# Optimization experiments

Measured on AMD Instinct MI355X. Metric: run time of the kernel, lower is better.

## Reference

```python
import jax, jax.numpy as jnp
import numpy as np

VOCAB = 32000
DIM = 1024
LAYERS = 4
B = 4
L = 1024


def setup_inputs() -> dict:
    key = jax.random.key(0)
    ks = jax.random.split(key, 5)
    input_ids = jax.random.randint(ks[0], (B, L), 0, VOCAB)
    embed = jax.random.normal(ks[1], (VOCAB, DIM), jnp.float32) * 0.02
    # 1/sqrt(fan_in) scaling keeps the recurrent state numerically stable over L steps
    W = jax.random.normal(ks[2], (LAYERS, 2 * DIM, 2 * DIM), jnp.float32) * (1.0 / np.sqrt(2 * DIM))
    out_w = jax.random.normal(ks[3], (VOCAB, DIM), jnp.float32) * 0.02
    starter = jax.random.normal(ks[4], (LAYERS, DIM), jnp.float32) * 0.02
    return {"input_ids": input_ids, "embed": embed, "W": W, "out_w": out_w, "starter": starter}


def reference(input_ids, embed, W, out_w, starter):
    Bsz, Lsz = input_ids.shape
    d = starter.shape[1]
    x = embed[input_ids]  # [B, L, d]
    # initial per-layer state, broadcast over batch: [layers, B, d]
    s0 = jnp.broadcast_to(starter[:, None, :], (W.shape[0], Bsz, d))

    def time_step(s_stack, x_t):
        # s_stack: [layers, B, d], x_t: [B, d]
        def layer_step(h, ws):
            Wi, si = ws  # Wi: [2d, 2d], si: [B, d]
            out = jnp.concatenate([h, si], axis=-1) @ Wi.T  # [B, 2d]
            h_new, s_new = jnp.split(out, 2, axis=-1)
            return h_new, s_new
        y, new_s = jax.lax.scan(layer_step, x_t, (W, s_stack))
        return new_s, y

    _, ys = jax.lax.scan(time_step, s0, jnp.swapaxes(x, 0, 1))  # ys: [L, B, d]
    logits = jnp.einsum('lbd,vd->blv', ys, out_w)  # [B, L, vocab]
    return logits
```

## Files before the change

### kernel.cpp

```cpp
#include <hip/hip_runtime.h>
#include <hip/hip_bf16.h>
#include <stdint.h>

#define BATCH 4
#define SEQ 1024
#define DIMX 1024
#define VOCAB 32000
#define NLAYERS 4
#define NBLK 256

#define W_GARR 4096
#define W_GREL 4608
#define W_LREL 4864
#define W_FLAG 5120

using bf16x8 = __attribute__((ext_vector_type(8))) short;
using f32x4v = __attribute__((ext_vector_type(4))) float;

__device__ __forceinline__ uint16_t f2b(float f) {
  __hip_bfloat16 h = __float2bfloat16(f);
  return *reinterpret_cast<uint16_t*>(&h);
}
__device__ __forceinline__ float b2f(uint16_t u) {
  __hip_bfloat16 h = *reinterpret_cast<__hip_bfloat16*>(&u);
  return __bfloat162float(h);
}
__device__ __forceinline__ void fsplit(float v, uint16_t& h, uint16_t& l) {
  h = f2b(v);
  l = f2b(v - b2f(h));
}

__device__ __forceinline__ uint32_t get_xcc() {
  uint32_t x;
  asm volatile("s_getreg_b32 %0, hwreg(HW_REG_XCC_ID)" : "=s"(x));
  return x & 7u;
}

__global__ __launch_bounds__(256) void k_embed_split(const int* __restrict__ ids,
                                                     const float* __restrict__ emb,
                                                     uint16_t* __restrict__ Hhi,
                                                     uint16_t* __restrict__ Hlo) {
  int idx = blockIdx.x * 256 + threadIdx.x;
  int d4 = idx & (DIMX / 4 - 1);
  int tb = idx >> 8;
  int t = tb >> 2, b = tb & 3;
  int id = ids[b * SEQ + t];
  float4 v = reinterpret_cast<const float4*>(emb + (size_t)id * DIMX)[d4];
  ushort4 h, l;
  fsplit(v.x, h.x, l.x); fsplit(v.y, h.y, l.y); fsplit(v.z, h.z, l.z); fsplit(v.w, h.w, l.w);
  reinterpret_cast<ushort4*>(Hhi)[idx] = h;
  reinterpret_cast<ushort4*>(Hlo)[idx] = l;
}

__global__ __launch_bounds__(256) void k_split_w(const float* __restrict__ W,
                                                 uint16_t* __restrict__ W1h, uint16_t* __restrict__ W1l,
                                                 uint16_t* __restrict__ WSh, uint16_t* __restrict__ WSl,
                                                 uint16_t* __restrict__ M1h, uint16_t* __restrict__ M1l) {
  int idx = blockIdx.x * 256 + threadIdx.x;
  int c4 = idx & 255;
  int row = idx >> 8;
  int l = row >> 12, r = row & 4095;
  const float* Wl = W + (size_t)l * 4 * 1024 * 1024;
  const float* src;
  uint16_t *dh, *dl;
  size_t doff;
  if (r < 2048) { src = Wl + (size_t)r * 2048; dh = W1h; dl = W1l; doff = ((size_t)l * 2048 + r) * 1024; }
  else if (r < 3072) { int rr = r - 2048; src = Wl + (size_t)rr * 2048 + 1024; dh = WSh; dl = WSl; doff = ((size_t)l * 1024 + rr) * 1024; }
  else { int rr = r - 3072; src = Wl + (size_t)(1024 + rr) * 2048 + 1024; dh = M1h; dl = M1l; doff = ((size_t)l * 1024 + rr) * 1024; }
  float4 v = reinterpret_cast<const float4*>(src)[c4];
  ushort4 h, lo4;
  fsplit(v.x, h.x, lo4.x); fsplit(v.y, h.y, lo4.y); fsplit(v.z, h.z, lo4.z); fsplit(v.w, h.w, lo4.w);
  reinterpret_cast<ushort4*>(dh + doff)[c4] = h;
  reinterpret_cast<ushort4*>(dl + doff)[c4] = lo4;
}

__global__ __launch_bounds__(256) void k_trans_w(const float* __restrict__ W,
                                                 uint16_t* __restrict__ T1h, uint16_t* __restrict__ T1l) {
  __shared__ float t[64][65];
  int l = blockIdx.z;
  const float* Wl = W + (size_t)l * 4 * 1024 * 1024;
  int i0 = blockIdx.y * 64, j0 = blockIdx.x * 64;
  int c4 = (threadIdx.x & 15) * 4, rr = threadIdx.x >> 4;
#pragma unroll
  for (int p = 0; p < 4; ++p) {
    int r = rr + p * 16;
    float4 v = *reinterpret_cast<const float4*>(Wl + (size_t)(1024 + i0 + r) * 2048 + 1024 + j0 + c4);
    t[r][c4] = v.x; t[r][c4 + 1] = v.y; t[r][c4 + 2] = v.z; t[r][c4 + 3] = v.w;
  }
  __syncthreads();
#pragma unroll
  for (int p = 0; p < 4; ++p) {
    int j = rr + p * 16;
    ushort4 h, l4;
    fsplit(t[c4 + 0][j], h.x, l4.x);
    fsplit(t[c4 + 1][j], h.y, l4.y);
    fsplit(t[c4 + 2][j], h.z, l4.z);
    fsplit(t[c4 + 3][j], h.w, l4.w);
    size_t o = (size_t)l * 1024 * 1024 + (size_t)(j0 + j) * 1024 + i0 + c4;
    *reinterpret_cast<ushort4*>(T1h + o) = h;
    *reinterpret_cast<ushort4*>(T1l + o) = l4;
  }
}

template <int BM, int BN>
__global__ __launch_bounds__(256) void k_mfma(
    int K,
    const uint16_t* __restrict__ Ahi, const uint16_t* __restrict__ Alo, int a_cs, int a_bs, size_t a_z,
    const uint16_t* __restrict__ Bhi, const uint16_t* __restrict__ Blo, int ldb, size_t b_z,
    const float* __restrict__ ADD, int add_cs, int add_bs,
    float* __restrict__ O1f, int o1_cs, int o1_bs,
    uint16_t* __restrict__ O1hi, uint16_t* __restrict__ O1lo, int o1s_cs, int o1s_bs, int split_n0, size_t o1_z,
    uint16_t* __restrict__ O2hi, uint16_t* __restrict__ O2lo, int o2_cs, int o2_bs, size_t o2_z) {
  constexpr int FM = BM / 32;
  constexpr int FN = BN / 32;
  __shared__ uint16_t sAh[BM * 32], sAl[BM * 32], sBh[BN * 32], sBl[BN * 32];
  size_t zb = blockIdx.z;
  Ahi += zb * a_z; Alo += zb * a_z;
  Bhi += zb * b_z; Blo += zb * b_z;
  if (O1hi) { O1hi += zb * o1_z; O1lo += zb * o1_z; }
  if (O2hi) { O2hi += zb * o2_z; O2lo += zb * o2_z; }
  int tid = threadIdx.x;
  int lane = tid & 63;
  int wave = tid >> 6;
  int wm = wave >> 1, wn = wave & 1;
  int m0 = blockIdx.y * BM, n0 = blockIdx.x * BN;
  f32x4v acc[FM][FN] = {};
  for (int kt = 0; kt < K; kt += 32) {
    __syncthreads();
#pragma unroll
    for (int q = 0; q < BM / 64; ++q) {
      int off = q * 4096 + tid * 16;
      int r = off >> 6;
      int cu = (off & 63) >> 1;
      size_t goff = (size_t)(m0 / 4 + (r >> 2)) * a_cs + (size_t)(r & 3) * a_bs + kt + cu;
      __builtin_amdgcn_global_load_lds(
          (const __attribute__((address_space(1))) uint32_t*)(Ahi + goff),
          (__attribute__((address_space(3))) uint32_t*)((char*)sAh + off), 16, 0, 0);
      __builtin_amdgcn_global_load_lds(
          (const __attribute__((address_space(1))) uint32_t*)(Alo + goff),
          (__attribute__((address_space(3))) uint32_t*)((char*)sAl + off), 16, 0, 0);
    }
#pragma unroll
    for (int q = 0; q < BN / 64; ++q) {
      int off = q * 4096 + tid * 16;
      int r = off >> 6, cu = (off & 63) >> 1;
      size_t goff = (size_t)(n0 + r) * ldb + kt + cu;
      __builtin_amdgcn_global_load_lds(
          (const __attribute__((address_space(1))) uint32_t*)(Bhi + goff),
          (__attribute__((address_space(3))) uint32_t*)((char*)sBh + off), 16, 0, 0);
      __builtin_amdgcn_global_load_lds(
          (const __attribute__((address_space(1))) uint32_t*)(Blo + goff),
          (__attribute__((address_space(3))) uint32_t*)((char*)sBl + off), 16, 0, 0);
    }
    __syncthreads();
    int rsel = lane & 15, ko = (lane >> 4) * 8;
    bf16x8 ah[FM], al[FM], bh[FN], bl[FN];
#pragma unroll
    for (int mf = 0; mf < FM; ++mf) {
      int row = wm * (FM * 16) + mf * 16 + rsel;
      ah[mf] = *reinterpret_cast<const bf16x8*>(sAh + row * 32 + ko);
      al[mf] = *reinterpret_cast<const bf16x8*>(sAl + row * 32 + ko);
    }
#pragma unroll
    for (int nf = 0; nf < FN; ++nf) {
      int row = wn * (FN * 16) + nf * 16 + rsel;
      bh[nf] = *reinterpret_cast<const bf16x8*>(sBh + row * 32 + ko);
      bl[nf] = *reinterpret_cast<const bf16x8*>(sBl + row * 32 + ko);
    }
#pragma unroll
    for (int mf = 0; mf < FM; ++mf)
#pragma unroll
      for (int nf = 0; nf < FN; ++nf) {
        acc[mf][nf] = __builtin_amdgcn_mfma_f32_16x16x32_bf16(ah[mf], bh[nf], acc[mf][nf], 0, 0, 0);
        acc[mf][nf] = __builtin_amdgcn_mfma_f32_16x16x32_bf16(ah[mf], bl[nf], acc[mf][nf], 0, 0, 0);
        acc[mf][nf] = __builtin_amdgcn_mfma_f32_16x16x32_bf16(al[mf], bh[nf], acc[mf][nf], 0, 0, 0);
      }
  }
  int rowg = (lane >> 4) * 4, colg = lane & 15;
#pragma unroll
  for (int mf = 0; mf < FM; ++mf)
#pragma unroll
    for (int nf = 0; nf < FN; ++nf)
#pragma unroll
      for (int r = 0; r < 4; ++r) {
        int m = m0 + wm * (FM * 16) + mf * 16 + rowg + r;
        int n = n0 + wn * (FN * 16) + nf * 16 + colg;
        size_t ro = (size_t)(m >> 2);
        float dot = acc[mf][nf][r];
        float v = dot;
        if (ADD) v += ADD[ro * add_cs + (size_t)(m & 3) * add_bs + n];
        if (O1f) O1f[ro * o1_cs + (size_t)(m & 3) * o1_bs + n] = v;
        if (O1hi && n >= split_n0) {
          uint16_t h, l;
          fsplit(v, h, l);
          size_t o = ro * o1s_cs + (size_t)(m & 3) * o1s_bs + (n - split_n0);
          O1hi[o] = h; O1lo[o] = l;
        }
        if (O2hi) {
          uint16_t h, l;
          fsplit(dot, h, l);
          size_t o = (o2_bs == 0) ? ((size_t)n * o2_cs + m)
                                  : (ro * o2_cs + (size_t)(m & 3) * o2_bs + n);
          O2hi[o] = h; O2lo[o] = l;
        }
      }
}

__device__ __forceinline__ void gbar(uint32_t* S, int flat, uint32_t& gen) {
  __syncthreads();
  gen++;
  int bid = blockIdx.x;
  if (flat) {
    if (threadIdx.x == 0)
      __hip_atomic_store(S + (size_t)bid * 16, gen, __ATOMIC_RELEASE, __HIP_MEMORY_SCOPE_AGENT);
    if (bid == 0) {
      while (__hip_atomic_load(S + (size_t)threadIdx.x * 16, __ATOMIC_RELAXED, __HIP_MEMORY_SCOPE_AGENT) < gen)
        __builtin_amdgcn_s_sleep(2);
      __syncthreads();
      if (threadIdx.x == 0) {
        __builtin_amdgcn_fence(__ATOMIC_ACQUIRE, "agent");
        __hip_atomic_store(S + W_GREL, gen, __ATOMIC_RELEASE, __HIP_MEMORY_SCOPE_AGENT);
      }
      __syncthreads();
    } else {
      if (threadIdx.x == 0) {
        while (__hip_atomic_load(S + W_GREL, __ATOMIC_RELAXED, __HIP_MEMORY_SCOPE_AGENT) < gen)
          __builtin_amdgcn_s_sleep(2);
        __builtin_amdgcn_fence(__ATOMIC_ACQUIRE, "agent");
      }
      __syncthreads();
    }
  } else {
    int xcd = bid & 7, q = bid >> 3;
    if (q != 0) {
      if (threadIdx.x == 0) {
        asm volatile("s_waitcnt vmcnt(0)" ::: "memory");
        __hip_atomic_store(S + (size_t)(xcd * 32 + q) * 16, gen, __ATOMIC_RELAXED, __HIP_MEMORY_SCOPE_AGENT);
        while (__hip_atomic_load(S + W_LREL + xcd * 16, __ATOMIC_RELAXED, __HIP_MEMORY_SCOPE_AGENT) < gen)
          __builtin_amdgcn_s_sleep(1);
        asm volatile("buffer_inv sc0" ::: "memory");
      }
      __builtin_amdgcn_sched_barrier(0);
      __syncthreads();
    } else {
      if (threadIdx.x < 31) {
        uint32_t* s = S + (size_t)(xcd * 32 + 1 + threadIdx.x) * 16;
        while (__hip_atomic_load(s, __ATOMIC_RELAXED, __HIP_MEMORY_SCOPE_AGENT) < gen)
          __builtin_amdgcn_s_sleep(1);
      }
      __syncthreads();
      if (threadIdx.x == 0)
        __hip_atomic_store(S + W_GARR + xcd * 16, gen, __ATOMIC_RELEASE, __HIP_MEMORY_SCOPE_AGENT);
      if (xcd == 0) {
        if (threadIdx.x < 8) {
          while (__hip_atomic_load(S + W_GARR + threadIdx.x * 16, __ATOMIC_RELAXED, __HIP_MEMORY_SCOPE_AGENT) < gen)
            __builtin_amdgcn_s_sleep(1);
        }
        __syncthreads();
        if (threadIdx.x == 0)
          __hip_atomic_store(S + W_GREL, gen, __ATOMIC_RELEASE, __HIP_MEMORY_SCOPE_AGENT);
      }
      if (threadIdx.x == 0) {
        while (__hip_atomic_load(S + W_GREL, __ATOMIC_RELAXED, __HIP_MEMORY_SCOPE_AGENT) < gen)
          __builtin_amdgcn_s_sleep(1);
        __builtin_amdgcn_fence(__ATOMIC_ACQUIRE, "agent");
        __hip_atomic_store(S + W_LREL + xcd * 16, gen, __ATOMIC_RELEASE, __HIP_MEMORY_SCOPE_AGENT);
      }
      __builtin_amdgcn_sched_barrier(0);
      __syncthreads();
    }
  }
}

__device__ __forceinline__ f32x4v wtile16(
    const uint16_t* __restrict__ Ah, const uint16_t* __restrict__ Al,
    int a_cs, int a_bs, int m0,
    const uint16_t* __restrict__ Bh, const uint16_t* __restrict__ Bl,
    int n0, int lane) {
  int rsel = lane & 15, ko = (lane >> 4) * 8;
  int am = m0 + rsel;
  const uint16_t* pah = Ah + (size_t)(am >> 2) * a_cs + (size_t)(am & 3) * a_bs + ko;
  const uint16_t* pal = Al + (size_t)(am >> 2) * a_cs + (size_t)(am & 3) * a_bs + ko;
  const uint16_t* pbh = Bh + (size_t)(n0 + rsel) * 1024 + ko;
  const uint16_t* pbl = Bl + (size_t)(n0 + rsel) * 1024 + ko;
  f32x4v acc = {0.f, 0.f, 0.f, 0.f};
#pragma unroll 4
  for (int kt = 0; kt < 1024; kt += 32) {
    bf16x8 ah = *reinterpret_cast<const bf16x8*>(pah + kt);
    bf16x8 al = *reinterpret_cast<const bf16x8*>(pal + kt);
    bf16x8 bh = *reinterpret_cast<const bf16x8*>(pbh + kt);
    bf16x8 bl = *reinterpret_cast<const bf16x8*>(pbl + kt);
    acc = __builtin_amdgcn_mfma_f32_16x16x32_bf16(ah, bh, acc, 0, 0, 0);
    acc = __builtin_amdgcn_mfma_f32_16x16x32_bf16(ah, bl, acc, 0, 0, 0);
    acc = __builtin_amdgcn_mfma_f32_16x16x32_bf16(al, bh, acc, 0, 0, 0);
  }
  return acc;
}

__device__ __forceinline__ f32x4v wtile16_lds(
    const uint16_t* __restrict__ Ah, const uint16_t* __restrict__ Al,
    int a_cs, int a_bs, int m0,
    const uint16_t* sBh, const uint16_t* sBl,
    int lane) {
  int rsel = lane & 15, ko = (lane >> 4) * 8;
  int am = m0 + rsel;
  const uint16_t* pah = Ah + (size_t)(am >> 2) * a_cs + (size_t)(am & 3) * a_bs + ko;
  const uint16_t* pal = Al + (size_t)(am >> 2) * a_cs + (size_t)(am & 3) * a_bs + ko;
  int rb = rsel * 1024;
  int s7 = rsel & 7;
  f32x4v acc0 = {0.f, 0.f, 0.f, 0.f}, acc1 = {0.f, 0.f, 0.f, 0.f};
#pragma unroll 4
  for (int kt = 0; kt < 1024; kt += 64) {
    int e0 = kt + ko, e1 = kt + 32 + ko;
    int o0 = rb + ((((e0) >> 3) ^ s7) << 3);
    int o1 = rb + ((((e1) >> 3) ^ s7) << 3);
    bf16x8 ah0 = *reinterpret_cast<const bf16x8*>(pah + kt);
    bf16x8 al0 = *reinterpret_cast<const bf16x8*>(pal + kt);
    bf16x8 ah1 = *reinterpret_cast<const bf16x8*>(pah + kt + 32);
    bf16x8 al1 = *reinterpret_cast<const bf16x8*>(pal + kt + 32);
    bf16x8 bh0 = *reinterpret_cast<const bf16x8*>(sBh + o0);
    bf16x8 bl0 = *reinterpret_cast<const bf16x8*>(sBl + o0);
    bf16x8 bh1 = *reinterpret_cast<const bf16x8*>(sBh + o1);
    bf16x8 bl1 = *reinterpret_cast<const bf16x8*>(sBl + o1);
    acc0 = __builtin_amdgcn_mfma_f32_16x16x32_bf16(ah0, bh0, acc0, 0, 0, 0);
    acc1 = __builtin_amdgcn_mfma_f32_16x16x32_bf16(ah1, bh1, acc1, 0, 0, 0);
    acc0 = __builtin_amdgcn_mfma_f32_16x16x32_bf16(ah0, bl0, acc0, 0, 0, 0);
    acc1 = __builtin_amdgcn_mfma_f32_16x16x32_bf16(ah1, bl1, acc1, 0, 0, 0);
    acc0 = __builtin_amdgcn_mfma_f32_16x16x32_bf16(al0, bh0, acc0, 0, 0, 0);
    acc1 = __builtin_amdgcn_mfma_f32_16x16x32_bf16(al1, bh1, acc1, 0, 0, 0);
  }
  return acc0 + acc1;
}

__global__ __launch_bounds__(256) void k_layer(
    uint32_t* S,
    float* __restrict__ P,
    uint16_t* __restrict__ PUh, uint16_t* __restrict__ PUl,
    uint16_t* __restrict__ Sh, uint16_t* __restrict__ Sl,
    const uint16_t* __restrict__ M1h, const uint16_t* __restrict__ M1l,
    const uint16_t* __restrict__ M16h, const uint16_t* __restrict__ M16l,
    const uint16_t* __restrict__ M128h, const uint16_t* __restrict__ M128l,
    uint16_t* G3h0, uint16_t* G3l0, uint16_t* G3h1, uint16_t* G3l1,
    uint16_t* BEh, uint16_t* BEl,
    float* LAMf, uint16_t* LAMh, uint16_t* LAMl,
    uint16_t* GSh0, uint16_t* GSl0, uint16_t* GSh1, uint16_t* GSl1,
    const float* __restrict__ starterL) {
  __shared__ uint16_t sB[2][32 * 1024];
  int tid = threadIdx.x, bid = blockIdx.x;
  int lane = tid & 63;
  int wv = tid >> 6;
  int xcd = bid & 7;
  int q = bid >> 3;
  uint32_t gen = 0;
  int rowg = (lane >> 4) * 4, colg = lane & 15;

  int nt13 = xcd * 8 + (q & 7);
  int m0_13 = ((q >> 3) * 4 + wv) * 16;
  int n0_13 = nt13 * 16;
  int m0_2 = (wv & 1) * 16;
  int nt2 = xcd * 8 + q * 2 + (wv >> 1);
  int n0_2 = nt2 * 16;
  int lrb2 = (wv >> 1) * 16 * 1024;
  int n0_b = (xcd * 8 + q * 4 + wv) * 16;

  {
    int idx = bid * 256 + tid;
    if (idx < BATCH * DIMX) {
      int b = idx >> 10, d = idx & 1023;
      float v = starterL[d];
      uint16_t h, l;
      fsplit(v, h, l);
      size_t o = (size_t)b * 1024 + d;
      BEh[o] = h; BEl[o] = l;
      G3h0[o] = h; G3l0[o] = l;
      GSh0[o] = h; GSl0[o] = l;
      Sh[o] = h; Sl[o] = l;
    }
  }

  if (threadIdx.x == 0 && get_xcc() != (uint32_t)xcd)
    __hip_atomic_store(S + W_FLAG, 1u, __ATOMIC_RELAXED, __HIP_MEMORY_SCOPE_AGENT);
  gbar(S, 1, gen);
  int flat = (int)__hip_atomic_load(S + W_FLAG, __ATOMIC_RELAXED, __HIP_MEMORY_SCOPE_AGENT);

  {
    const uint16_t* gh = M1h + (size_t)n0_13 * 1024;
    const uint16_t* gl = M1l + (size_t)n0_13 * 1024;
    for (int i = tid; i < 16 * 128; i += 256) {
      int r = i >> 7, c8 = i & 127;
      int dst = r * 1024 + ((c8 ^ (r & 7)) << 3);
      *reinterpret_cast<bf16x8*>(&sB[0][dst]) = *reinterpret_cast<const bf16x8*>(gh + (size_t)r * 1024 + c8 * 8);
      *reinterpret_cast<bf16x8*>(&sB[1][dst]) = *reinterpret_cast<const bf16x8*>(gl + (size_t)r * 1024 + c8 * 8);
    }
  }
  __syncthreads();

  for (int j = 1; j < 16; ++j) {
    {
      f32x4v acc = wtile16_lds(PUh + (size_t)(j - 1) * 4096, PUl + (size_t)(j - 1) * 4096,
                               65536, 1024, m0_13, &sB[0][0], &sB[1][0], lane);
      int n = n0_13 + colg;
#pragma unroll
      for (int rr = 0; rr < 4; ++rr) {
        int m = m0_13 + rowg + rr;
        int c = m >> 2, b = m & 3;
        size_t t = (size_t)(c * 16 + j);
        float* pu = P + (t * 4 + b) * 2048 + 1024 + n;
        float v = acc[rr] + *pu;
        *pu = v;
        uint16_t h, l;
        fsplit(v, h, l);
        size_t o = (t * 4 + b) * 1024 + n;
        PUh[o] = h; PUl[o] = l;
      }
    }
    gbar(S, flat, gen);
  }

  {
    int idx = bid * 256 + tid;
    if (idx < 32 * 1024) {
      int r = idx >> 10, d = idx & 1023;
      int g = r >> 2, b = r & 3;
      float v = P[((size_t)(g * 128 + 15) * 4 + b) * 2048 + 1024 + d];
      LAMf[idx] = v;
      uint16_t h, l;
      fsplit(v, h, l);
      LAMh[idx] = h; LAMl[idx] = l;
    }
  }
  gbar(S, flat, gen);

  if (q < 4) {
    int nb = (xcd * 8 + q * 2) * 16;
    const uint16_t* gh = M16h + (size_t)nb * 1024;
    const uint16_t* gl = M16l + (size_t)nb * 1024;
    for (int i = tid; i < 32 * 128; i += 256) {
      int r = i >> 7, c8 = i & 127;
      int dst = r * 1024 + ((c8 ^ (r & 7)) << 3);
      *reinterpret_cast<bf16x8*>(&sB[0][dst]) = *reinterpret_cast<const bf16x8*>(gh + (size_t)r * 1024 + c8 * 8);
      *reinterpret_cast<bf16x8*>(&sB[1][dst]) = *reinterpret_cast<const bf16x8*>(gl + (size_t)r * 1024 + c8 * 8);
    }
  }
  __syncthreads();

  for (int j = 1; j < 8; ++j) {
    if (q < 4) {
      f32x4v acc = wtile16_lds(LAMh + (size_t)(j - 1) * 32768, LAMl + (size_t)(j - 1) * 32768,
                               4096, 1024, m0_2, &sB[0][lrb2], &sB[1][lrb2], lane);
      int n = n0_2 + colg;
#pragma unroll
      for (int rr = 0; rr < 4; ++rr) {
        int m = m0_2 + rowg + rr;
        int g = m >> 2, b = m & 3;
        int c = 8 * g + j;
        float e = P[((size_t)(c * 16 + 15) * 4 + b) * 2048 + 1024 + n];
        float v = acc[rr] + e;
        size_t o = (size_t)j * 32768 + (size_t)m * 1024 + n;
        LAMf[o] = v;
        uint16_t h, l;
        fsplit(v, h, l);
        LAMh[o] = h; LAMl[o] = l;
      }
    }
    gbar(S, flat, gen);
  }

  for (int g = 0; g < 7; ++g) {
    if (q < 2) {
      f32x4v acc = wtile16(BEh + (size_t)g * 16384, BEl + (size_t)g * 16384,
                           4096, 1024, 0, M128h, M128l, n0_b, lane);
      if ((lane >> 4) == 0) {
        int n = n0_b + colg;
#pragma unroll
        for (int rr = 0; rr < 4; ++rr) {
          int b = rr;
          float v = acc[rr] + LAMf[(size_t)7 * 32768 + (size_t)(g * 4 + b) * 1024 + n];
          uint16_t h, l;
          fsplit(v, h, l);
          size_t ob = (size_t)(g + 1) * 16384 + (size_t)b * 1024 + n;
          BEh[ob] = h; BEl[ob] = l;
          int c = 8 * (g + 1);
          size_t o1 = (size_t)(c * 4 + b) * 1024 + n;
          G3h0[o1] = h; G3l0[o1] = l;
          size_t o2 = ((size_t)(c * 16) * 4 + b) * 1024 + n;
          Sh[o2] = h; Sl[o2] = l;
          size_t o3 = (size_t)((g + 1) * 4 + b) * 1024 + n;
          GSh0[o3] = h; GSl0[o3] = l;
        }
      }
    }
    gbar(S, flat, gen);
  }

  int gsc = 0;
  for (int j = 1; j < 8; ++j) {
    uint16_t* gih = gsc ? GSh1 : GSh0;
    uint16_t* gil = gsc ? GSl1 : GSl0;
    uint16_t* goh = gsc ? GSh0 : GSh1;
    uint16_t* gol = gsc ? GSl0 : GSl1;
    if (q < 4) {
      f32x4v acc = wtile16_lds(gih, gil, 4096, 1024, m0_2, &sB[0][lrb2], &sB[1][lrb2], lane);
      int n = n0_2 + colg;
#pragma unroll
      for (int rr = 0; rr < 4; ++rr) {
        int m = m0_2 + rowg + rr;
        int g = m >> 2, b = m & 3;
        int c = 8 * g + j;
        float lam = LAMf[(size_t)(j - 1) * 32768 + (size_t)m * 1024 + n];
        float v = acc[rr] + lam;
        uint16_t h, l;
        fsplit(v, h, l);
        size_t o1 = (size_t)(c * 4 + b) * 1024 + n;
        G3h0[o1] = h; G3l0[o1] = l;
        size_t o2 = ((size_t)(c * 16) * 4 + b) * 1024 + n;
        Sh[o2] = h; Sl[o2] = l;
        uint16_t h2, l2;
        fsplit(acc[rr], h2, l2);
        goh[(size_t)m * 1024 + n] = h2;
        gol[(size_t)m * 1024 + n] = l2;
      }
    }
    gbar(S, flat, gen);
    gsc ^= 1;
  }

  {
    const uint16_t* gh = M1h + (size_t)n0_13 * 1024;
    const uint16_t* gl = M1l + (size_t)n0_13 * 1024;
    for (int i = tid; i < 16 * 128; i += 256) {
      int r = i >> 7, c8 = i & 127;
      int dst = r * 1024 + ((c8 ^ (r & 7)) << 3);
      *reinterpret_cast<bf16x8*>(&sB[0][dst]) = *reinterpret_cast<const bf16x8*>(gh + (size_t)r * 1024 + c8 * 8);
      *reinterpret_cast<bf16x8*>(&sB[1][dst]) = *reinterpret_cast<const bf16x8*>(gl + (size_t)r * 1024 + c8 * 8);
    }
  }
  __syncthreads();

  int g3 = 0;
  for (int j = 1; j < 16; ++j) {
    uint16_t* gih = g3 ? G3h1 : G3h0;
    uint16_t* gil = g3 ? G3l1 : G3l0;
    uint16_t* goh = g3 ? G3h0 : G3h1;
    uint16_t* gol = g3 ? G3l0 : G3l1;
    {
      f32x4v acc = wtile16_lds(gih, gil, 4096, 1024, m0_13, &sB[0][0], &sB[1][0], lane);
      int n = n0_13 + colg;
#pragma unroll
      for (int rr = 0; rr < 4; ++rr) {
        int m = m0_13 + rowg + rr;
        int c = m >> 2, b = m & 3;
        float u = P[((size_t)(c * 16 + j - 1) * 4 + b) * 2048 + 1024 + n];
        float v = acc[rr] + u;
        uint16_t h, l;
        fsplit(v, h, l);
        size_t o = ((size_t)(c * 16 + j) * 4 + b) * 1024 + n;
        Sh[o] = h; Sl[o] = l;
        uint16_t h2, l2;
        fsplit(acc[rr], h2, l2);
        goh[(size_t)m * 1024 + n] = h2;
        gol[(size_t)m * 1024 + n] = l2;
      }
    }
    if (j < 15) gbar(S, flat, gen);
    g3 ^= 1;
  }
}

__global__ __launch_bounds__(256) void k_reorder_hi(const uint16_t* __restrict__ Hhi, uint16_t* __restrict__ Y) {
  int idx = blockIdx.x * 256 + threadIdx.x;
  int d4 = idx & (DIMX / 4 - 1);
  int tb = idx >> 8;
  int t = tb >> 2, b = tb & 3;
  ushort4 v = reinterpret_cast<const ushort4*>(Hhi)[idx];
  reinterpret_cast<ushort4*>(Y + (size_t)(b * SEQ + t) * DIMX)[d4] = v;
}

__global__ __launch_bounds__(256) void k_cast_w(const float* __restrict__ src, uint16_t* __restrict__ dst, int n4) {
  int idx = blockIdx.x * 256 + threadIdx.x;
  if (idx >= n4) return;
  float4 v = reinterpret_cast<const float4*>(src)[idx];
  ushort4 o;
  o.x = f2b(v.x); o.y = f2b(v.y); o.z = f2b(v.z); o.w = f2b(v.w);
  reinterpret_cast<ushort4*>(dst)[idx] = o;
}

__global__ __launch_bounds__(256) void k_logits(const uint16_t* __restrict__ A,
                                                const uint16_t* __restrict__ Bt,
                                                float* __restrict__ C) {
  __shared__ uint16_t As[128 * 32];
  __shared__ uint16_t Bs[128 * 32];
  int tid = threadIdx.x;
  int bx = blockIdx.x, by = blockIdx.y;
  int lane = tid & 63, wave = tid >> 6;
  int wm = wave >> 1, wn = wave & 1;
  f32x4v acc[4][4] = {};
  const uint16_t* Ag = A + (size_t)by * 128 * 1024;
  const uint16_t* Bg = Bt + (size_t)bx * 128 * 1024;
  for (int kt = 0; kt < 1024; kt += 32) {
    __syncthreads();
#pragma unroll
    for (int q = 0; q < 2; ++q) {
      int off = q * 4096 + tid * 16;
      int r = off >> 6, cu = (off & 63) >> 1;
      __builtin_amdgcn_global_load_lds(
          (const __attribute__((address_space(1))) uint32_t*)(Ag + (size_t)r * 1024 + kt + cu),
          (__attribute__((address_space(3))) uint32_t*)((char*)As + off), 16, 0, 0);
      __builtin_amdgcn_global_load_lds(
          (const __attribute__((address_space(1))) uint32_t*)(Bg + (size_t)r * 1024 + kt + cu),
          (__attribute__((address_space(3))) uint32_t*)((char*)Bs + off), 16, 0, 0);
    }
    __syncthreads();
    int rsel = lane & 15, ko = (lane >> 4) * 8;
    bf16x8 af[4], bfr[4];
#pragma unroll
    for (int mf = 0; mf < 4; ++mf)
      af[mf] = *reinterpret_cast<const bf16x8*>(As + (wm * 64 + mf * 16 + rsel) * 32 + ko);
#pragma unroll
    for (int nf = 0; nf < 4; ++nf)
      bfr[nf] = *reinterpret_cast<const bf16x8*>(Bs + (wn * 64 + nf * 16 + rsel) * 32 + ko);
#pragma unroll
    for (int mf = 0; mf < 4; ++mf)
#pragma unroll
      for (int nf = 0; nf < 4; ++nf)
        acc[mf][nf] = __builtin_amdgcn_mfma_f32_16x16x32_bf16(af[mf], bfr[nf], acc[mf][nf], 0, 0, 0);
  }
  int rowg = (lane >> 4) * 4;
  int colg = lane & 15;
#pragma unroll
  for (int mf = 0; mf < 4; ++mf)
#pragma unroll
    for (int nf = 0; nf < 4; ++nf)
#pragma unroll
      for (int r = 0; r < 4; ++r) {
        int m = by * 128 + wm * 64 + mf * 16 + rowg + r;
        int n = bx * 128 + wn * 64 + nf * 16 + colg;
        C[(size_t)m * VOCAB + n] = acc[mf][nf][r];
      }
}

extern "C" void kernel_launch(void* const* d_in, const int* in_sizes, int n_in,
                              void* d_out, int out_size, void* d_ws, size_t ws_size,
                              hipStream_t stream) {
  const int* ids = (const int*)d_in[0];
  const float* emb = (const float*)d_in[1];
  const float* W = (const float*)d_in[2];
  const float* outw = (const float*)d_in[3];
  const float* starter = (const float*)d_in[4];
  float* out = (float*)d_out;

  char* wsb = (char*)d_ws;
  size_t off = 0;
  auto alloc = [&](size_t bytes) {
    void* p = wsb + off;
    off = (off + bytes + 255) & ~(size_t)255;
    return p;
  };
  const size_t TB = SEQ * BATCH;
  const size_t MB1 = (size_t)1024 * 1024;

  uint32_t* SYNC = (uint32_t*)alloc((size_t)NLAYERS * 8192 * 4);
  uint16_t* Hh[2] = {(uint16_t*)alloc(TB * DIMX * 2), (uint16_t*)alloc(TB * DIMX * 2)};
  uint16_t* Hl[2] = {(uint16_t*)alloc(TB * DIMX * 2), (uint16_t*)alloc(TB * DIMX * 2)};
  float* P = (float*)alloc(TB * 2 * DIMX * 4);
  uint16_t* PUh = (uint16_t*)alloc(TB * DIMX * 2);
  uint16_t* PUl = (uint16_t*)alloc(TB * DIMX * 2);
  uint16_t* Sh = (uint16_t*)alloc(TB * DIMX * 2);
  uint16_t* Sl = (uint16_t*)alloc(TB * DIMX * 2);
  uint16_t* W1h = (uint16_t*)alloc((size_t)NLAYERS * 2048 * 1024 * 2);
  uint16_t* W1l = (uint16_t*)alloc((size_t)NLAYERS * 2048 * 1024 * 2);
  uint16_t* WSh = (uint16_t*)alloc((size_t)NLAYERS * MB1 * 2);
  uint16_t* WSl = (uint16_t*)alloc((size_t)NLAYERS * MB1 * 2);
  uint16_t* M1h = (uint16_t*)alloc((size_t)NLAYERS * MB1 * 2);
  uint16_t* M1l = (uint16_t*)alloc((size_t)NLAYERS * MB1 * 2);
  uint16_t* T1h = (uint16_t*)alloc((size_t)NLAYERS * MB1 * 2);
  uint16_t* T1l = (uint16_t*)alloc((size_t)NLAYERS * MB1 * 2);
  uint16_t* M16Ah = (uint16_t*)alloc((size_t)NLAYERS * MB1 * 2);
  uint16_t* M16Al = (uint16_t*)alloc((size_t)NLAYERS * MB1 * 2);
  uint16_t* M128Ah = (uint16_t*)alloc((size_t)NLAYERS * MB1 * 2);
  uint16_t* M128Al = (uint16_t*)alloc((size_t)NLAYERS * MB1 * 2);
  uint16_t* G3h0 = (uint16_t*)alloc((size_t)256 * 1024 * 2);
  uint16_t* G3l0 = (uint16_t*)alloc((size_t)256 * 1024 * 2);
  uint16_t* G3h1 = (uint16_t*)alloc((size_t)256 * 1024 * 2);
  uint16_t* G3l1 = (uint16_t*)alloc((size_t)256 * 1024 * 2);
  uint16_t* BEh = (uint16_t*)alloc((size_t)8 * 16 * 1024 * 2);
  uint16_t* BEl = (uint16_t*)alloc((size_t)8 * 16 * 1024 * 2);
  float* LAMf = (float*)alloc((size_t)8 * 32 * 1024 * 4);
  uint16_t* LAMh = (uint16_t*)alloc((size_t)8 * 32 * 1024 * 2);
  uint16_t* LAMl = (uint16_t*)alloc((size_t)8 * 32 * 1024 * 2);
  uint16_t* GSh0 = (uint16_t*)alloc((size_t)32 * 1024 * 2);
  uint16_t* GSl0 = (uint16_t*)alloc((size_t)32 * 1024 * 2);
  uint16_t* GSh1 = (uint16_t*)alloc((size_t)32 * 1024 * 2);
  uint16_t* GSl1 = (uint16_t*)alloc((size_t)32 * 1024 * 2);
  uint16_t* YSB = (uint16_t*)alloc(TB * DIMX * 2);
  uint16_t* OWB = (uint16_t*)alloc((size_t)VOCAB * DIMX * 2);

  uint16_t* CMh[2] = {(uint16_t*)P, Sh};
  uint16_t* CMl[2] = {(uint16_t*)P + 4 * MB1, Sl};
  uint16_t* CTh[2] = {(uint16_t*)P + 8 * MB1, Hh[1]};
  uint16_t* CTl[2] = {(uint16_t*)P + 12 * MB1, Hl[1]};

  hipMemsetAsync(SYNC, 0, (size_t)NLAYERS * 8192 * 4, stream);
  k_split_w<<<NLAYERS * 4096, 256, 0, stream>>>(W, W1h, W1l, WSh, WSl, M1h, M1l);
  k_trans_w<<<dim3(16, 16, NLAYERS), 256, 0, stream>>>(W, T1h, T1l);
  k_cast_w<<<(int)((size_t)VOCAB * DIMX / 4 / 256), 256, 0, stream>>>(outw, OWB, VOCAB * DIMX / 4);
  k_embed_split<<<(int)(TB * DIMX / 4 / 256), 256, 0, stream>>>(ids, emb, Hh[0], Hl[0]);

  {
    const uint16_t *inMh = M1h, *inMl = M1l, *inTh = T1h, *inTl = T1l;
    for (int k = 1; k <= 7; ++k) {
      uint16_t *oMh, *oMl;
      if (k == 4) { oMh = M16Ah; oMl = M16Al; }
      else if (k == 7) { oMh = M128Ah; oMl = M128Al; }
      else { oMh = CMh[k & 1]; oMl = CMl[k & 1]; }
      uint16_t* oTh = (k < 7) ? CTh[k & 1] : nullptr;
      uint16_t* oTl = (k < 7) ? CTl[k & 1] : nullptr;
      k_mfma<128, 128><<<dim3(8, 8, NLAYERS), 256, 0, stream>>>(
          1024,
          inMh, inMl, 4096, 1024, MB1,
          inTh, inTl, 1024, MB1,
          nullptr, 0, 0,
          nullptr, 0, 0,
          oMh, oMl, 4096, 1024, 0, MB1,
          oTh, oTl, 1024, 0, MB1);
      inMh = oMh; inMl = oMl; inTh = oTh; inTl = oTl;
    }
  }

  int cur = 0;
  for (int l = 0; l < NLAYERS; ++l) {
    k_mfma<128, 128><<<dim3(16, 32, 1), 256, 0, stream>>>(
        1024,
        Hh[cur], Hl[cur], 4096, 1024, 0,
        W1h + (size_t)l * 2048 * 1024, W1l + (size_t)l * 2048 * 1024, 1024, 0,
        nullptr, 0, 0,
        P, 8192, 2048,
        PUh, PUl, 4096, 1024, 1024, 0,
        nullptr, nullptr, 0, 1, 0);

    k_layer<<<NBLK, 256, 0, stream>>>(
        SYNC + (size_t)l * 8192,
        P, PUh, PUl, Sh, Sl,
        M1h + (size_t)l * MB1, M1l + (size_t)l * MB1,
        M16Ah + (size_t)l * MB1, M16Al + (size_t)l * MB1,
        M128Ah + (size_t)l * MB1, M128Al + (size_t)l * MB1,
        G3h0, G3l0, G3h1, G3l1,
        BEh, BEl, LAMf, LAMh, LAMl,
        GSh0, GSl0, GSh1, GSl1,
        starter + (size_t)l * DIMX);

    k_mfma<128, 128><<<dim3(8, 32, 1), 256, 0, stream>>>(
        1024,
        Sh, Sl, 4096, 1024, 0,
        WSh + (size_t)l * MB1, WSl + (size_t)l * MB1, 1024, 0,
        P, 8192, 2048,
        nullptr, 0, 0,
        Hh[cur ^ 1], Hl[cur ^ 1], 4096, 1024, 0, 0,
        nullptr, nullptr, 0, 1, 0);
    cur ^= 1;
  }

  k_reorder_hi<<<(int)(TB * DIMX / 4 / 256), 256, 0, stream>>>(Hh[cur], YSB);
  k_logits<<<dim3(VOCAB / 128, TB / 128), 256, 0, stream>>>(YSB, OWB, out);
}
```

Measured before the change: 4.229 ms.

## Localize scan stages per XCD and use XCD-local barriers between steps

```diff
diff --git a/kernel.cpp b/kernel.cpp
--- a/kernel.cpp
+++ b/kernel.cpp
@@ -206,35 +206,36 @@
       }
 }
 
-__device__ __forceinline__ void gbar(uint32_t* S, int flat, uint32_t& gen) {
+__device__ __forceinline__ void bar_any(uint32_t* S, int flat, int global, uint32_t& gen) {
+  gen++;
   __syncthreads();
-  gen++;
-  int bid = blockIdx.x;
+  int bid = blockIdx.x, tid = threadIdx.x;
   if (flat) {
-    if (threadIdx.x == 0)
+    if (tid == 0)
       __hip_atomic_store(S + (size_t)bid * 16, gen, __ATOMIC_RELEASE, __HIP_MEMORY_SCOPE_AGENT);
     if (bid == 0) {
-      while (__hip_atomic_load(S + (size_t)threadIdx.x * 16, __ATOMIC_RELAXED, __HIP_MEMORY_SCOPE_AGENT) < gen)
+      while (__hip_atomic_load(S + (size_t)tid * 16, __ATOMIC_RELAXED, __HIP_MEMORY_SCOPE_AGENT) < gen)
         __builtin_amdgcn_s_sleep(2);
       __syncthreads();
-      if (threadIdx.x == 0) {
+      if (tid == 0) {
         __builtin_amdgcn_fence(__ATOMIC_ACQUIRE, "agent");
         __hip_atomic_store(S + W_GREL, gen, __ATOMIC_RELEASE, __HIP_MEMORY_SCOPE_AGENT);
       }
       __syncthreads();
     } else {
-      if (threadIdx.x == 0) {
+      if (tid == 0) {
         while (__hip_atomic_load(S + W_GREL, __ATOMIC_RELAXED, __HIP_MEMORY_SCOPE_AGENT) < gen)
           __builtin_amdgcn_s_sleep(2);
         __builtin_amdgcn_fence(__ATOMIC_ACQUIRE, "agent");
       }
       __syncthreads();
     }
-  } else {
-    int xcd = bid & 7, q = bid >> 3;
+    return;
+  }
+  int xcd = bid & 7, q = bid >> 3;
+  if (global) {
     if (q != 0) {
-      if (threadIdx.x == 0) {
-        asm volatile("s_waitcnt vmcnt(0)" ::: "memory");
+      if (tid == 0) {
         __hip_atomic_store(S + (size_t)(xcd * 32 + q) * 16, gen, __ATOMIC_RELAXED, __HIP_MEMORY_SCOPE_AGENT);
         while (__hip_atomic_load(S + W_LREL + xcd * 16, __ATOMIC_RELAXED, __HIP_MEMORY_SCOPE_AGENT) < gen)
           __builtin_amdgcn_s_sleep(1);
@@ -243,28 +244,52 @@
       __builtin_amdgcn_sched_barrier(0);
       __syncthreads();
     } else {
-      if (threadIdx.x < 31) {
-        uint32_t* s = S + (size_t)(xcd * 32 + 1 + threadIdx.x) * 16;
+      if (tid < 31) {
+        uint32_t* s = S + (size_t)(xcd * 32 + 1 + tid) * 16;
         while (__hip_atomic_load(s, __ATOMIC_RELAXED, __HIP_MEMORY_SCOPE_AGENT) < gen)
           __builtin_amdgcn_s_sleep(1);
       }
       __syncthreads();
-      if (threadIdx.x == 0)
+      if (tid == 0)
         __hip_atomic_store(S + W_GARR + xcd * 16, gen, __ATOMIC_RELEASE, __HIP_MEMORY_SCOPE_AGENT);
       if (xcd == 0) {
-        if (threadIdx.x < 8) {
-          while (__hip_atomic_load(S + W_GARR + threadIdx.x * 16, __ATOMIC_RELAXED, __HIP_MEMORY_SCOPE_AGENT) < gen)
+        if (tid < 8) {
+          while (__hip_atomic_load(S + W_GARR + tid * 16, __ATOMIC_RELAXED, __HIP_MEMORY_SCOPE_AGENT) < gen)
             __builtin_amdgcn_s_sleep(1);
         }
         __syncthreads();
-        if (threadIdx.x == 0)
+        if (tid == 0)
           __hip_atomic_store(S + W_GREL, gen, __ATOMIC_RELEASE, __HIP_MEMORY_SCOPE_AGENT);
       }
-      if (threadIdx.x == 0) {
+      if (tid == 0) {
         while (__hip_atomic_load(S + W_GREL, __ATOMIC_RELAXED, __HIP_MEMORY_SCOPE_AGENT) < gen)
           __builtin_amdgcn_s_sleep(1);
         __builtin_amdgcn_fence(__ATOMIC_ACQUIRE, "agent");
         __hip_atomic_store(S + W_LREL + xcd * 16, gen, __ATOMIC_RELEASE, __HIP_MEMORY_SCOPE_AGENT);
+      }
+      __builtin_amdgcn_sched_barrier(0);
+      __syncthreads();
+    }
+  } else {
+    if (q != 0) {
+      if (tid == 0) {
+        __hip_atomic_store(S + (size_t)(xcd * 32 + q) * 16, gen, __ATOMIC_RELAXED, __HIP_MEMORY_SCOPE_AGENT);
+        while (__hip_atomic_load(S + W_LREL + xcd * 16, __ATOMIC_RELAXED, __HIP_MEMORY_SCOPE_AGENT) < gen)
+          __builtin_amdgcn_s_sleep(1);
+        asm volatile("buffer_inv sc0" ::: "memory");
+      }
+      __builtin_amdgcn_sched_barrier(0);
+      __syncthreads();
+    } else {
+      if (tid < 31) {
+        uint32_t* s = S + (size_t)(xcd * 32 + 1 + tid) * 16;
+        while (__hip_atomic_load(s, __ATOMIC_RELAXED, __HIP_MEMORY_SCOPE_AGENT) < gen)
+          __builtin_amdgcn_s_sleep(1);
+      }
+      __syncthreads();
+      if (tid == 0) {
+        asm volatile("buffer_inv sc0" ::: "memory");
+        __hip_atomic_store(S + W_LREL + xcd * 16, gen, __ATOMIC_RELAXED, __HIP_MEMORY_SCOPE_AGENT);
       }
       __builtin_amdgcn_sched_barrier(0);
       __syncthreads();
@@ -354,14 +379,10 @@
   uint32_t gen = 0;
   int rowg = (lane >> 4) * 4, colg = lane & 15;
 
-  int nt13 = xcd * 8 + (q & 7);
-  int m0_13 = ((q >> 3) * 4 + wv) * 16;
-  int n0_13 = nt13 * 16;
-  int m0_2 = (wv & 1) * 16;
-  int nt2 = xcd * 8 + q * 2 + (wv >> 1);
-  int n0_2 = nt2 * 16;
-  int lrb2 = (wv >> 1) * 16 * 1024;
-  int n0_b = (xcd * 8 + q * 4 + wv) * 16;
+  int m0_13 = xcd * 32 + (wv & 1) * 16;
+  int n0_13 = (2 * q + (wv >> 1)) * 16;
+  int lrb13 = (wv >> 1) * 16 * 1024;
+  int n0_2 = (q * 4 + wv) * 16;
 
   {
     int idx = bid * 256 + tid;
@@ -378,15 +399,15 @@
     }
   }
 
-  if (threadIdx.x == 0 && get_xcc() != (uint32_t)xcd)
+  if (tid == 0 && get_xcc() != (uint32_t)xcd)
     __hip_atomic_store(S + W_FLAG, 1u, __ATOMIC_RELAXED, __HIP_MEMORY_SCOPE_AGENT);
-  gbar(S, 1, gen);
+  bar_any(S, 1, 1, gen);
   int flat = (int)__hip_atomic_load(S + W_FLAG, __ATOMIC_RELAXED, __HIP_MEMORY_SCOPE_AGENT);
 
   {
-    const uint16_t* gh = M1h + (size_t)n0_13 * 1024;
-    const uint16_t* gl = M1l + (size_t)n0_13 * 1024;
-    for (int i = tid; i < 16 * 128; i += 256) {
+    const uint16_t* gh = M1h + (size_t)(32 * q) * 1024;
+    const uint16_t* gl = M1l + (size_t)(32 * q) * 1024;
+    for (int i = tid; i < 32 * 128; i += 256) {
       int r = i >> 7, c8 = i & 127;
       int dst = r * 1024 + ((c8 ^ (r & 7)) << 3);
       *reinterpret_cast<bf16x8*>(&sB[0][dst]) = *reinterpret_cast<const bf16x8*>(gh + (size_t)r * 1024 + c8 * 8);
@@ -398,7 +419,7 @@
   for (int j = 1; j < 16; ++j) {
     {
       f32x4v acc = wtile16_lds(PUh + (size_t)(j - 1) * 4096, PUl + (size_t)(j - 1) * 4096,
-                               65536, 1024, m0_13, &sB[0][0], &sB[1][0], lane);
+                               65536, 1024, m0_13, &sB[0][lrb13], &sB[1][lrb13], lane);
       int n = n0_13 + colg;
 #pragma unroll
       for (int rr = 0; rr < 4; ++rr) {
@@ -414,68 +435,55 @@
         PUh[o] = h; PUl[o] = l;
       }
     }
-    gbar(S, flat, gen);
-  }
-
-  {
-    int idx = bid * 256 + tid;
-    if (idx < 32 * 1024) {
-      int r = idx >> 10, d = idx & 1023;
-      int g = r >> 2, b = r & 3;
-      float v = P[((size_t)(g * 128 + 15) * 4 + b) * 2048 + 1024 + d];
-      LAMf[idx] = v;
+    bar_any(S, flat, 0, gen);
+  }
+
+  if (q == 0) {
+    for (int i = tid; i < 4096; i += 256) {
+      int b = i >> 10, d = i & 1023;
+      float v = P[((size_t)(xcd * 128 + 15) * 4 + b) * 2048 + 1024 + d];
+      size_t o = (size_t)xcd * 16384 + (size_t)b * 1024 + d;
+      LAMf[o] = v;
       uint16_t h, l;
       fsplit(v, h, l);
-      LAMh[idx] = h; LAMl[idx] = l;
-    }
-  }
-  gbar(S, flat, gen);
-
-  if (q < 4) {
-    int nb = (xcd * 8 + q * 2) * 16;
-    const uint16_t* gh = M16h + (size_t)nb * 1024;
-    const uint16_t* gl = M16l + (size_t)nb * 1024;
-    for (int i = tid; i < 32 * 128; i += 256) {
-      int r = i >> 7, c8 = i & 127;
-      int dst = r * 1024 + ((c8 ^ (r & 7)) << 3);
-      *reinterpret_cast<bf16x8*>(&sB[0][dst]) = *reinterpret_cast<const bf16x8*>(gh + (size_t)r * 1024 + c8 * 8);
-      *reinterpret_cast<bf16x8*>(&sB[1][dst]) = *reinterpret_cast<const bf16x8*>(gl + (size_t)r * 1024 + c8 * 8);
-    }
-  }
-  __syncthreads();
+      LAMh[o] = h; LAMl[o] = l;
+    }
+  }
+  bar_any(S, flat, 0, gen);
 
   for (int j = 1; j < 8; ++j) {
-    if (q < 4) {
-      f32x4v acc = wtile16_lds(LAMh + (size_t)(j - 1) * 32768, LAMl + (size_t)(j - 1) * 32768,
-                               4096, 1024, m0_2, &sB[0][lrb2], &sB[1][lrb2], lane);
-      int n = n0_2 + colg;
-#pragma unroll
-      for (int rr = 0; rr < 4; ++rr) {
-        int m = m0_2 + rowg + rr;
-        int g = m >> 2, b = m & 3;
-        int c = 8 * g + j;
-        float e = P[((size_t)(c * 16 + 15) * 4 + b) * 2048 + 1024 + n];
-        float v = acc[rr] + e;
-        size_t o = (size_t)j * 32768 + (size_t)m * 1024 + n;
-        LAMf[o] = v;
-        uint16_t h, l;
-        fsplit(v, h, l);
-        LAMh[o] = h; LAMl[o] = l;
-      }
-    }
-    gbar(S, flat, gen);
-  }
-
-  for (int g = 0; g < 7; ++g) {
-    if (q < 2) {
-      f32x4v acc = wtile16(BEh + (size_t)g * 16384, BEl + (size_t)g * 16384,
-                           4096, 1024, 0, M128h, M128l, n0_b, lane);
-      if ((lane >> 4) == 0) {
-        int n = n0_b + colg;
+    if (q < 16) {
+      size_t abase = (size_t)(j - 1) * 131072 + (size_t)xcd * 16384;
+      f32x4v acc = wtile16(LAMh + abase, LAMl + abase, 4096, 1024, 0, M16h, M16l, n0_2, lane);
+      if (rowg == 0) {
+        int n = n0_2 + colg;
 #pragma unroll
         for (int rr = 0; rr < 4; ++rr) {
           int b = rr;
-          float v = acc[rr] + LAMf[(size_t)7 * 32768 + (size_t)(g * 4 + b) * 1024 + n];
+          int c = 8 * xcd + j;
+          float e = P[((size_t)(c * 16 + 15) * 4 + b) * 2048 + 1024 + n];
+          float v = acc[rr] + e;
+          size_t o = (size_t)j * 131072 + (size_t)xcd * 16384 + (size_t)b * 1024 + n;
+          LAMf[o] = v;
+          uint16_t h, l;
+          fsplit(v, h, l);
+          LAMh[o] = h; LAMl[o] = l;
+        }
+      }
+    }
+    bar_any(S, flat, (j == 7) ? 1 : 0, gen);
+  }
+
+  for (int g = 0; g < 7; ++g) {
+    if (xcd == 0 && q < 16) {
+      f32x4v acc = wtile16(BEh + (size_t)g * 16384, BEl + (size_t)g * 16384,
+                           4096, 1024, 0, M128h, M128l, n0_2, lane);
+      if (rowg == 0) {
+        int n = n0_2 + colg;
+#pragma unroll
+        for (int rr = 0; rr < 4; ++rr) {
+          int b = rr;
+          float v = acc[rr] + LAMf[(size_t)7 * 131072 + (size_t)g * 16384 + (size_t)b * 1024 + n];
           uint16_t h, l;
           fsplit(v, h, l);
           size_t ob = (size_t)(g + 1) * 16384 + (size_t)b * 1024 + n;
@@ -485,12 +493,11 @@
           G3h0[o1] = h; G3l0[o1] = l;
           size_t o2 = ((size_t)(c * 16) * 4 + b) * 1024 + n;
           Sh[o2] = h; Sl[o2] = l;
-          size_t o3 = (size_t)((g + 1) * 4 + b) * 1024 + n;
-          GSh0[o3] = h; GSl0[o3] = l;
+          GSh0[ob] = h; GSl0[ob] = l;
         }
       }
     }
-    gbar(S, flat, gen);
+    bar_any(S, flat, (g == 6) ? 1 : 0, gen);
   }
 
   int gsc = 0;
@@ -499,43 +506,33 @@
     uint16_t* gil = gsc ? GSl1 : GSl0;
     uint16_t* goh = gsc ? GSh0 : GSh1;
     uint16_t* gol = gsc ? GSl0 : GSl1;
-    if (q < 4) {
-      f32x4v acc = wtile16_lds(gih, gil, 4096, 1024, m0_2, &sB[0][lrb2], &sB[1][lrb2], lane);
-      int n = n0_2 + colg;
-#pragma unroll
-      for (int rr = 0; rr < 4; ++rr) {
-        int m = m0_2 + rowg + rr;
-        int g = m >> 2, b = m & 3;
-        int c = 8 * g + j;
-        float lam = LAMf[(size_t)(j - 1) * 32768 + (size_t)m * 1024 + n];
-        float v = acc[rr] + lam;
-        uint16_t h, l;
-        fsplit(v, h, l);
-        size_t o1 = (size_t)(c * 4 + b) * 1024 + n;
-        G3h0[o1] = h; G3l0[o1] = l;
-        size_t o2 = ((size_t)(c * 16) * 4 + b) * 1024 + n;
-        Sh[o2] = h; Sl[o2] = l;
-        uint16_t h2, l2;
-        fsplit(acc[rr], h2, l2);
-        goh[(size_t)m * 1024 + n] = h2;
-        gol[(size_t)m * 1024 + n] = l2;
-      }
-    }
-    gbar(S, flat, gen);
+    if (q < 16) {
+      size_t gbase = (size_t)xcd * 16384;
+      f32x4v acc = wtile16(gih + gbase, gil + gbase, 4096, 1024, 0, M16h, M16l, n0_2, lane);
+      if (rowg == 0) {
+        int n = n0_2 + colg;
+#pragma unroll
+        for (int rr = 0; rr < 4; ++rr) {
+          int b = rr;
+          int c = 8 * xcd + j;
+          float lam = LAMf[(size_t)(j - 1) * 131072 + (size_t)xcd * 16384 + (size_t)b * 1024 + n];
+          float v = acc[rr] + lam;
+          uint16_t h, l;
+          fsplit(v, h, l);
+          size_t o1 = (size_t)(c * 4 + b) * 1024 + n;
+          G3h0[o1] = h; G3l0[o1] = l;
+          size_t o2 = ((size_t)(c * 16) * 4 + b) * 1024 + n;
+          Sh[o2] = h; Sl[o2] = l;
+          uint16_t h2, l2;
+          fsplit(acc[rr], h2, l2);
+          goh[gbase + (size_t)b * 1024 + n] = h2;
+          gol[gbase + (size_t)b * 1024 + n] = l2;
+        }
+      }
+    }
+    bar_any(S, flat, 0, gen);
     gsc ^= 1;
   }
-
-  {
-    const uint16_t* gh = M1h + (size_t)n0_13 * 1024;
-    const uint16_t* gl = M1l + (size_t)n0_13 * 1024;
-    for (int i = tid; i < 16 * 128; i += 256) {
-      int r = i >> 7, c8 = i & 127;
-      int dst = r * 1024 + ((c8 ^ (r & 7)) << 3);
-      *reinterpret_cast<bf16x8*>(&sB[0][dst]) = *reinterpret_cast<const bf16x8*>(gh + (size_t)r * 1024 + c8 * 8);
-      *reinterpret_cast<bf16x8*>(&sB[1][dst]) = *reinterpret_cast<const bf16x8*>(gl + (size_t)r * 1024 + c8 * 8);
-    }
-  }
-  __syncthreads();
 
   int g3 = 0;
   for (int j = 1; j < 16; ++j) {
@@ -544,7 +541,7 @@
     uint16_t* goh = g3 ? G3h0 : G3h1;
     uint16_t* gol = g3 ? G3l0 : G3l1;
     {
-      f32x4v acc = wtile16_lds(gih, gil, 4096, 1024, m0_13, &sB[0][0], &sB[1][0], lane);
+      f32x4v acc = wtile16_lds(gih, gil, 4096, 1024, m0_13, &sB[0][lrb13], &sB[1][lrb13], lane);
       int n = n0_13 + colg;
 #pragma unroll
       for (int rr = 0; rr < 4; ++rr) {
@@ -562,7 +559,7 @@
         gol[(size_t)m * 1024 + n] = l2;
       }
     }
-    if (j < 15) gbar(S, flat, gen);
+    if (j < 15) bar_any(S, flat, 0, gen);
     g3 ^= 1;
   }
 }
@@ -685,13 +682,13 @@
   uint16_t* G3l1 = (uint16_t*)alloc((size_t)256 * 1024 * 2);
   uint16_t* BEh = (uint16_t*)alloc((size_t)8 * 16 * 1024 * 2);
   uint16_t* BEl = (uint16_t*)alloc((size_t)8 * 16 * 1024 * 2);
-  float* LAMf = (float*)alloc((size_t)8 * 32 * 1024 * 4);
-  uint16_t* LAMh = (uint16_t*)alloc((size_t)8 * 32 * 1024 * 2);
-  uint16_t* LAMl = (uint16_t*)alloc((size_t)8 * 32 * 1024 * 2);
-  uint16_t* GSh0 = (uint16_t*)alloc((size_t)32 * 1024 * 2);
-  uint16_t* GSl0 = (uint16_t*)alloc((size_t)32 * 1024 * 2);
-  uint16_t* GSh1 = (uint16_t*)alloc((size_t)32 * 1024 * 2);
-  uint16_t* GSl1 = (uint16_t*)alloc((size_t)32 * 1024 * 2);
+  float* LAMf = (float*)alloc((size_t)8 * 128 * 1024 * 4);
+  uint16_t* LAMh = (uint16_t*)alloc((size_t)8 * 128 * 1024 * 2);
+  uint16_t* LAMl = (uint16_t*)alloc((size_t)8 * 128 * 1024 * 2);
+  uint16_t* GSh0 = (uint16_t*)alloc((size_t)128 * 1024 * 2);
+  uint16_t* GSl0 = (uint16_t*)alloc((size_t)128 * 1024 * 2);
+  uint16_t* GSh1 = (uint16_t*)alloc((size_t)128 * 1024 * 2);
+  uint16_t* GSl1 = (uint16_t*)alloc((size_t)128 * 1024 * 2);
   uint16_t* YSB = (uint16_t*)alloc(TB * DIMX * 2);
   uint16_t* OWB = (uint16_t*)alloc((size_t)VOCAB * DIMX * 2);
 
```

After: 4.206 ms. No clear change (-0.6%).
